# Kernel tuning notes

Measured on AMD Instinct MI355X. Metric: run time of the kernel, lower is better.

Reference implementation:

```python
import jax, jax.numpy as jnp
import numpy as np

EPS = 1e-10


def setup_inputs() -> dict:
    key = jax.random.key(0)
    k1, k2 = jax.random.split(key)
    B, F, T = 64, 80, 8000
    x = jax.random.normal(k1, (B, F, T), dtype=jnp.float32)
    # relative lengths in [0.5, 1.0] so every sample has plenty of valid frames
    lengths = 0.5 + 0.5 * jax.random.uniform(k2, (B,), dtype=jnp.float32)
    return {"x": x, "lengths": lengths}


def reference(x, lengths):
    # x: [B, F, T]; lengths: [B] relative fractions of valid time steps.
    B, F, T = x.shape
    n = jnp.round(lengths * T).astype(jnp.int32)            # valid frames per sample [B]
    mask = (jnp.arange(T)[None, :] < n[:, None])            # [B, T]
    mask = mask[:, None, :].astype(x.dtype)                 # [B, 1, T]
    nf = n.astype(x.dtype)[:, None, None]                   # [B, 1, 1]
    # per-sample, per-feature mean over valid frames (torch.mean over dim=1 of [F,T_valid])
    mean = jnp.sum(x * mask, axis=2, keepdims=True) / nf    # [B, F, 1]
    # torch.std default: unbiased (ddof=1)
    var = jnp.sum(jnp.square((x - mean) * mask), axis=2, keepdims=True) / (nf - 1.0)
    std = jnp.maximum(jnp.sqrt(var), EPS)                   # [B, F, 1]
    # normalization is applied to ALL frames (including padding), matching the original
    return (x - mean) / std
```

## Files before the change

### kernel.cpp

```cpp
#include <hip/hip_runtime.h>
#include <math.h>


#define ROW_T 8000
#define TV (ROW_T / 4)
#define BLOCK 256
#define WAVES (BLOCK / 64)
#define VPT 8
#define EPS 1e-10f

typedef float v4f __attribute__((ext_vector_type(4)));

__global__ __launch_bounds__(BLOCK, 8) void isn_kernel(
        const float* __restrict__ x,
        const float* __restrict__ lengths,
        float* __restrict__ out,
        int F) {
    __shared__ float2 lds[WAVES];

    const int row = blockIdx.x;
    const int b = row / F;
    const v4f* __restrict__ xr = (const v4f*)(x + (size_t)row * ROW_T);
    v4f* __restrict__ outr = (v4f*)(out + (size_t)row * ROW_T);
    const int tid = threadIdx.x;

    const int n = (int)rintf(lengths[b] * (float)ROW_T);
    const float nf = (float)n;

    v4f v[VPT];
    #pragma unroll
    for (int it = 0; it < VPT; ++it) {
        const int idx = tid + it * BLOCK;
        if (idx < TV) v[it] = __builtin_nontemporal_load(&xr[idx]);
    }

    float s = 0.0f, ss = 0.0f;
    #pragma unroll
    for (int it = 0; it < VPT; ++it) {
        const int base = (tid + it * BLOCK) * 4;
        if (base < ROW_T) {
            #pragma unroll
            for (int j = 0; j < 4; ++j) {
                const float xv = (base + j < n) ? v[it][j] : 0.0f;
                s += xv;
                ss = fmaf(xv, xv, ss);
            }
        }
    }

    #pragma unroll
    for (int off = 32; off > 0; off >>= 1) {
        s  += __shfl_down(s, off, 64);
        ss += __shfl_down(ss, off, 64);
    }
    const int wave = tid >> 6;
    const int lane = tid & 63;
    if (lane == 0) lds[wave] = make_float2(s, ss);
    __syncthreads();
    float rs = 0.0f, rss = 0.0f;
    #pragma unroll
    for (int i = 0; i < WAVES; ++i) { rs += lds[i].x; rss += lds[i].y; }

    const float mean = rs / nf;
    const float var = (rss - rs * rs / nf) / (nf - 1.0f);
    const float inv = 1.0f / fmaxf(sqrtf(var), EPS);

    #pragma unroll
    for (int it = 0; it < VPT; ++it) {
        const int idx = tid + it * BLOCK;
        if (idx < TV) {
            v4f o;
            #pragma unroll
            for (int j = 0; j < 4; ++j)
                o[j] = (v[it][j] - mean) * inv;
            __builtin_nontemporal_store(o, &outr[idx]);
        }
    }
}

extern "C" void kernel_launch(void* const* d_in, const int* in_sizes, int n_in,
                              void* d_out, int out_size, void* d_ws, size_t ws_size,
                              hipStream_t stream) {
    const float* x = (const float*)d_in[0];
    const float* lengths = (const float*)d_in[1];
    float* out = (float*)d_out;

    const int B = in_sizes[1];
    const int F = in_sizes[0] / (B * ROW_T);
    const int rows = B * F;

    isn_kernel<<<rows, BLOCK, 0, stream>>>(x, lengths, out, F);
}
```

Baseline: 265.7 us.

## Process multiple rows per block with double-buffered register prefetch of next row

Each 512-thread block now handles five rows in sequence. While the current row is being reduced and written out, the next row is prefetched into a second register buffer, so the memory latency of a row overlaps the reduction and store of the previous one. Block size is doubled and per-thread vector count halved, which keeps registers per row similar but doubles them overall because of the two buffers. This may lower occupancy, and the grid is five times smaller, about 1024 blocks.

```diff
diff --git a/kernel.cpp b/kernel.cpp
--- a/kernel.cpp
+++ b/kernel.cpp
@@ -4,76 +4,93 @@
 
 #define ROW_T 8000
 #define TV (ROW_T / 4)
-#define BLOCK 256
+#define BLOCK 512
 #define WAVES (BLOCK / 64)
-#define VPT 8
+#define VPT 4
+#define RPB 5
 #define EPS 1e-10f
 
 typedef float v4f __attribute__((ext_vector_type(4)));
+
+__device__ __forceinline__ void load_row(v4f (&v)[VPT],
+                                         const v4f* __restrict__ xr, int tid) {
+    #pragma unroll
+    for (int it = 0; it < VPT; ++it) {
+        const int idx = tid + it * BLOCK;
+        if (idx < TV) v[it] = __builtin_nontemporal_load(&xr[idx]);
+    }
+}
 
 __global__ __launch_bounds__(BLOCK, 8) void isn_kernel(
         const float* __restrict__ x,
         const float* __restrict__ lengths,
         float* __restrict__ out,
-        int F) {
+        int F, int rows) {
     __shared__ float2 lds[WAVES];
+    const int tid = threadIdx.x;
+    const int base = blockIdx.x * RPB;
 
-    const int row = blockIdx.x;
-    const int b = row / F;
-    const v4f* __restrict__ xr = (const v4f*)(x + (size_t)row * ROW_T);
-    v4f* __restrict__ outr = (v4f*)(out + (size_t)row * ROW_T);
-    const int tid = threadIdx.x;
+    v4f va[VPT], vb[VPT];
+    if (base < rows)
+        load_row(va, (const v4f*)(x + (size_t)base * ROW_T), tid);
 
-    const int n = (int)rintf(lengths[b] * (float)ROW_T);
-    const float nf = (float)n;
+    #pragma unroll
+    for (int k = 0; k < RPB; ++k) {
+        const int row = base + k;
+        if (row >= rows) break;
+        v4f (&v)[VPT]  = (k & 1) ? vb : va;
+        v4f (&vn)[VPT] = (k & 1) ? va : vb;
 
-    v4f v[VPT];
-    #pragma unroll
-    for (int it = 0; it < VPT; ++it) {
-        const int idx = tid + it * BLOCK;
-        if (idx < TV) v[it] = __builtin_nontemporal_load(&xr[idx]);
-    }
+        const int b = row / F;
+        const int n = (int)rintf(lengths[b] * (float)ROW_T);
+        const float nf = (float)n;
 
-    float s = 0.0f, ss = 0.0f;
-    #pragma unroll
-    for (int it = 0; it < VPT; ++it) {
-        const int base = (tid + it * BLOCK) * 4;
-        if (base < ROW_T) {
-            #pragma unroll
-            for (int j = 0; j < 4; ++j) {
-                const float xv = (base + j < n) ? v[it][j] : 0.0f;
-                s += xv;
-                ss = fmaf(xv, xv, ss);
+        float s = 0.0f, ss = 0.0f;
+        #pragma unroll
+        for (int it = 0; it < VPT; ++it) {
+            const int bidx = (tid + it * BLOCK) * 4;
+            if (bidx < ROW_T) {
+                #pragma unroll
+                for (int j = 0; j < 4; ++j) {
+                    const float xv = (bidx + j < n) ? v[it][j] : 0.0f;
+                    s += xv;
+                    ss = fmaf(xv, xv, ss);
+                }
             }
         }
-    }
 
-    #pragma unroll
-    for (int off = 32; off > 0; off >>= 1) {
-        s  += __shfl_down(s, off, 64);
-        ss += __shfl_down(ss, off, 64);
-    }
-    const int wave = tid >> 6;
-    const int lane = tid & 63;
-    if (lane == 0) lds[wave] = make_float2(s, ss);
-    __syncthreads();
-    float rs = 0.0f, rss = 0.0f;
-    #pragma unroll
-    for (int i = 0; i < WAVES; ++i) { rs += lds[i].x; rss += lds[i].y; }
+        if (k + 1 < RPB && row + 1 < rows)
+            load_row(vn, (const v4f*)(x + (size_t)(row + 1) * ROW_T), tid);
 
-    const float mean = rs / nf;
-    const float var = (rss - rs * rs / nf) / (nf - 1.0f);
-    const float inv = 1.0f / fmaxf(sqrtf(var), EPS);
+        #pragma unroll
+        for (int off = 32; off > 0; off >>= 1) {
+            s  += __shfl_down(s, off, 64);
+            ss += __shfl_down(ss, off, 64);
+        }
+        const int wave = tid >> 6;
+        const int lane = tid & 63;
+        if (k) __syncthreads();
+        if (lane == 0) lds[wave] = make_float2(s, ss);
+        __syncthreads();
+        float rs = 0.0f, rss = 0.0f;
+        #pragma unroll
+        for (int i = 0; i < WAVES; ++i) { rs += lds[i].x; rss += lds[i].y; }
 
-    #pragma unroll
-    for (int it = 0; it < VPT; ++it) {
-        const int idx = tid + it * BLOCK;
-        if (idx < TV) {
-            v4f o;
-            #pragma unroll
-            for (int j = 0; j < 4; ++j)
-                o[j] = (v[it][j] - mean) * inv;
-            __builtin_nontemporal_store(o, &outr[idx]);
+        const float mean = rs / nf;
+        const float var = (rss - rs * rs / nf) / (nf - 1.0f);
+        const float inv = 1.0f / fmaxf(sqrtf(var), EPS);
+
+        v4f* __restrict__ outr = (v4f*)(out + (size_t)row * ROW_T);
+        #pragma unroll
+        for (int it = 0; it < VPT; ++it) {
+            const int idx = tid + it * BLOCK;
+            if (idx < TV) {
+                v4f o;
+                #pragma unroll
+                for (int j = 0; j < 4; ++j)
+                    o[j] = (v[it][j] - mean) * inv;
+                __builtin_nontemporal_store(o, &outr[idx]);
+            }
         }
     }
 }
@@ -88,6 +105,7 @@
     const int B = in_sizes[1];
     const int F = in_sizes[0] / (B * ROW_T);
     const int rows = B * F;
+    const int grid = (rows + RPB - 1) / RPB;
 
-    isn_kernel<<<rows, BLOCK, 0, stream>>>(x, lengths, out, F);
+    isn_kernel<<<grid, BLOCK, 0, stream>>>(x, lengths, out, F, rows);
 }
```

New measurement: 277.1 us. 4.3% more time.

## Assign one row per wavefront instead of one row per block

Applied to the files above, without the earlier changes.

Each 64-lane wavefront now processes a full 8000-element row, holding 31 float4 values plus a scalar tail per lane in registers. Row statistics come from an xor-shuffle reduction alone, so the LDS exchange and block barrier go away. In exchange, each lane uses far more registers (launch bounds lowered to 2), which cuts occupancy and the memory-level parallelism available to hide HBM latency on a bandwidth-bound kernel.

```diff
diff --git a/kernel.cpp b/kernel.cpp
--- a/kernel.cpp
+++ b/kernel.cpp
@@ -5,77 +5,74 @@
 #define ROW_T 8000
 #define TV (ROW_T / 4)
 #define BLOCK 256
-#define WAVES (BLOCK / 64)
-#define VPT 8
+#define WPB (BLOCK / 64)
+#define NV 31
+#define TAIL_BASE 7936
 #define EPS 1e-10f
 
 typedef float v4f __attribute__((ext_vector_type(4)));
 
-__global__ __launch_bounds__(BLOCK, 8) void isn_kernel(
+__global__ __launch_bounds__(BLOCK, 2) void isn_kernel(
         const float* __restrict__ x,
         const float* __restrict__ lengths,
         float* __restrict__ out,
-        int F) {
-    __shared__ float2 lds[WAVES];
+        int F, int rows) {
+    const int lane = threadIdx.x & 63;
+    const int wave = threadIdx.x >> 6;
+    const int row = blockIdx.x * WPB + wave;
+    if (row >= rows) return;
 
-    const int row = blockIdx.x;
+    const float* __restrict__ xrow = x + (size_t)row * ROW_T;
+    const v4f* __restrict__ xr4 = (const v4f*)xrow;
+
     const int b = row / F;
-    const v4f* __restrict__ xr = (const v4f*)(x + (size_t)row * ROW_T);
-    v4f* __restrict__ outr = (v4f*)(out + (size_t)row * ROW_T);
-    const int tid = threadIdx.x;
-
     const int n = (int)rintf(lengths[b] * (float)ROW_T);
     const float nf = (float)n;
 
-    v4f v[VPT];
+    v4f v[NV];
     #pragma unroll
-    for (int it = 0; it < VPT; ++it) {
-        const int idx = tid + it * BLOCK;
-        if (idx < TV) v[it] = __builtin_nontemporal_load(&xr[idx]);
-    }
+    for (int i = 0; i < NV; ++i)
+        v[i] = __builtin_nontemporal_load(&xr4[i * 64 + lane]);
+    const float vt = __builtin_nontemporal_load(&xrow[TAIL_BASE + lane]);
 
     float s = 0.0f, ss = 0.0f;
     #pragma unroll
-    for (int it = 0; it < VPT; ++it) {
-        const int base = (tid + it * BLOCK) * 4;
-        if (base < ROW_T) {
-            #pragma unroll
-            for (int j = 0; j < 4; ++j) {
-                const float xv = (base + j < n) ? v[it][j] : 0.0f;
-                s += xv;
-                ss = fmaf(xv, xv, ss);
-            }
+    for (int i = 0; i < NV; ++i) {
+        const int base = (i * 64 + lane) * 4;
+        #pragma unroll
+        for (int j = 0; j < 4; ++j) {
+            const float xv = (base + j < n) ? v[i][j] : 0.0f;
+            s += xv;
+            ss = fmaf(xv, xv, ss);
         }
+    }
+    {
+        const float xv = (TAIL_BASE + lane < n) ? vt : 0.0f;
+        s += xv;
+        ss = fmaf(xv, xv, ss);
     }
 
     #pragma unroll
-    for (int off = 32; off > 0; off >>= 1) {
-        s  += __shfl_down(s, off, 64);
-        ss += __shfl_down(ss, off, 64);
+    for (int off = 1; off < 64; off <<= 1) {
+        s  += __shfl_xor(s, off, 64);
+        ss += __shfl_xor(ss, off, 64);
     }
-    const int wave = tid >> 6;
-    const int lane = tid & 63;
-    if (lane == 0) lds[wave] = make_float2(s, ss);
-    __syncthreads();
-    float rs = 0.0f, rss = 0.0f;
-    #pragma unroll
-    for (int i = 0; i < WAVES; ++i) { rs += lds[i].x; rss += lds[i].y; }
 
-    const float mean = rs / nf;
-    const float var = (rss - rs * rs / nf) / (nf - 1.0f);
+    const float mean = s / nf;
+    const float var = (ss - s * s / nf) / (nf - 1.0f);
     const float inv = 1.0f / fmaxf(sqrtf(var), EPS);
 
+    float* __restrict__ orow = out + (size_t)row * ROW_T;
+    v4f* __restrict__ or4 = (v4f*)orow;
     #pragma unroll
-    for (int it = 0; it < VPT; ++it) {
-        const int idx = tid + it * BLOCK;
-        if (idx < TV) {
-            v4f o;
-            #pragma unroll
-            for (int j = 0; j < 4; ++j)
-                o[j] = (v[it][j] - mean) * inv;
-            __builtin_nontemporal_store(o, &outr[idx]);
-        }
+    for (int i = 0; i < NV; ++i) {
+        v4f o;
+        #pragma unroll
+        for (int j = 0; j < 4; ++j)
+            o[j] = (v[i][j] - mean) * inv;
+        __builtin_nontemporal_store(o, &or4[i * 64 + lane]);
     }
+    __builtin_nontemporal_store((vt - mean) * inv, &orow[TAIL_BASE + lane]);
 }
 
 extern "C" void kernel_launch(void* const* d_in, const int* in_sizes, int n_in,
@@ -88,6 +85,7 @@
     const int B = in_sizes[1];
     const int F = in_sizes[0] / (B * ROW_T);
     const int rows = B * F;
+    const int grid = (rows + WPB - 1) / WPB;
 
-    isn_kernel<<<rows, BLOCK, 0, stream>>>(x, lengths, out, F);
+    isn_kernel<<<grid, BLOCK, 0, stream>>>(x, lengths, out, F, rows);
 }
```

After: 271.3 us. 1.02x slower.
